# Kernel tuning notes

Hardware: AMD Instinct MI355X
Metric: run time of the kernel (lower is better)

The kernel has to match this reference:

```python
import jax, jax.numpy as jnp
import numpy as np

NUM_NODES = 50000
EMB_DIM = 128
PROJ_DIM = 768
HIDDEN = 256
NUM_REL = 16
NUM_BASES = 2
NUM_LAYERS = 3
NUM_EDGES = 400000
BN_EPS = 1e-5


def setup_inputs() -> dict:
    key = jax.random.key(0)
    ks = jax.random.split(key, 32)
    inp = {}
    inp["edge_index"] = jax.random.randint(ks[0], (2, NUM_EDGES), 0, NUM_NODES)
    inp["edge_type"] = jax.random.randint(ks[1], (NUM_EDGES,), 0, NUM_REL)
    inp["emb"] = jax.random.normal(ks[2], (NUM_NODES, EMB_DIM), jnp.float32)
    inp["proj_w"] = jax.random.normal(ks[3], (EMB_DIM, PROJ_DIM), jnp.float32) * 0.02
    inp["proj_b"] = jnp.zeros((PROJ_DIM,), jnp.float32)
    dims_in = [PROJ_DIM, HIDDEN, HIDDEN]
    for l in range(NUM_LAYERS):
        d_in = dims_in[l]
        k0, k1, k2 = jax.random.split(ks[4 + l], 3)
        inp[f"comp{l}"] = jax.random.normal(k0, (NUM_REL, NUM_BASES), jnp.float32)
        inp[f"bases{l}"] = jax.random.normal(k1, (NUM_BASES, d_in, HIDDEN), jnp.float32) * (1.0 / np.sqrt(d_in))
        inp[f"root{l}"] = jax.random.normal(k2, (d_in, HIDDEN), jnp.float32) * (1.0 / np.sqrt(d_in))
        inp[f"bias{l}"] = jnp.zeros((HIDDEN,), jnp.float32)
        inp[f"gamma{l}"] = jnp.ones((HIDDEN,), jnp.float32)
        inp[f"beta{l}"] = jnp.zeros((HIDDEN,), jnp.float32)
    return inp


def _rgcn_conv(x, src, dst, edge_type, comp, bases, root, bias):
    # Basis decomposition: W_r = sum_b comp[r,b] * bases[b]
    # Transform nodes per basis once: [B, N, out]
    h = jnp.einsum('nd,bdo->bno', x, bases)
    c = comp[edge_type]                         # [E, B]
    msg = jnp.einsum('beo,eb->eo', h[:, src, :], c)  # [E, out]
    # PyG RGCNConv uses mean aggregation per relation
    seg = dst * NUM_REL + edge_type             # combined (node, relation) id
    cnt = jax.ops.segment_sum(jnp.ones((msg.shape[0],), x.dtype), seg,
                              num_segments=NUM_NODES * NUM_REL)
    denom = jnp.maximum(cnt[seg], 1.0)
    agg = jax.ops.segment_sum(msg / denom[:, None], dst, num_segments=NUM_NODES)
    return agg + x @ root + bias


def _batchnorm(x, gamma, beta):
    mu = jnp.mean(x, axis=0)
    var = jnp.mean(jnp.square(x - mu), axis=0)  # biased, as in torch BN training
    return (x - mu) * jax.lax.rsqrt(var + BN_EPS) * gamma + beta


def reference(edge_index, edge_type, emb, proj_w, proj_b,
              comp0, bases0, root0, bias0, gamma0, beta0,
              comp1, bases1, root1, bias1, gamma1, beta1,
              comp2, bases2, root2, bias2, gamma2, beta2):
    src, dst = edge_index[0], edge_index[1]
    x = emb / jnp.maximum(jnp.linalg.norm(emb, axis=-1, keepdims=True), 1e-12)
    x = x @ proj_w + proj_b
    layers = [(comp0, bases0, root0, bias0, gamma0, beta0),
              (comp1, bases1, root1, bias1, gamma1, beta1),
              (comp2, bases2, root2, bias2, gamma2, beta2)]
    for (comp, bases, root, bias, gamma, beta) in layers:
        x = _rgcn_conv(x, src, dst, edge_type, comp, bases, root, bias)
        x = _batchnorm(x, gamma, beta)
        x = jax.nn.relu(x)
        # dropout: identity (eval mode / deterministic reference)
    return x
```

## Files before the change

kernel.cpp:

```cpp
#include <hip/hip_runtime.h>
#include <hip/hip_bf16.h>

#define NNODES 50000
#define NREL   16
#define NEDGE  400000
#define BN_EPS 1e-5f
#define M_REAL NNODES
#define MT256  196
#define SCAN_B 512
#define SCAN_NB ((NNODES + SCAN_B - 1) / SCAN_B)

typedef __attribute__((ext_vector_type(8))) short short8;
typedef __attribute__((ext_vector_type(4))) float f4;

__device__ __forceinline__ float bf2f(unsigned short u) {
    union { unsigned int i; float f; } x; x.i = ((unsigned int)u) << 16; return x.f;
}
__device__ __forceinline__ unsigned short f2bf(float f) {
    __hip_bfloat16 h = __float2bfloat16(f);
    union { __hip_bfloat16 h; unsigned short u; } x; x.h = h; return x.u;
}

__device__ __forceinline__ void g2l16(const unsigned short* g, unsigned short* l) {
    __builtin_amdgcn_global_load_lds(
        (const __attribute__((address_space(1))) unsigned int*)g,
        (__attribute__((address_space(3))) unsigned int*)l,
        16, 0, 0);
}

template<int K>
__global__ __launch_bounds__(512) void gemm3_k(
    const unsigned short* __restrict__ A,
    const unsigned short* __restrict__ WT,
    const float* __restrict__ bias,
    unsigned short* __restrict__ y,
    float* __restrict__ bns)
{
    const int tile_m = blockIdx.x * 256;

    __shared__ unsigned short As[2][256 * 64];
    __shared__ unsigned short Bs[2][256 * 64];

    const int w = threadIdx.x >> 6;
    const int l = threadIdx.x & 63;
    const int lm = l & 15;
    const int kq = l >> 4;
    const int wm = (w & 1) << 7;
    const int wn = (w >> 1) << 6;

    const int lrow = l >> 3;
    const int chunk = ((l & 7) + 8 - lrow) & 7;
    const unsigned short* srcA[4];
    const unsigned short* srcB[4];
    int dstoff[4];
#pragma unroll
    for (int it = 0; it < 4; ++it) {
        int rt = it * 64 + w * 8 + lrow;
        int rg = tile_m + rt; if (rg >= M_REAL) rg = M_REAL - 1;
        srcA[it] = A  + (size_t)rg * K + chunk * 8;
        srcB[it] = WT + (size_t)rt * K + chunk * 8;
        dstoff[it] = (it * 64 + w * 8) * 64;
    }

    unsigned aoff[8], boff[4];
#pragma unroll
    for (int mi = 0; mi < 8; ++mi)
        aoff[mi] = (unsigned)((wm + mi * 16 + lm) * 128 + (((kq + lm) & 7) << 4));
#pragma unroll
    for (int ni = 0; ni < 4; ++ni)
        boff[ni] = (unsigned)((wn + ni * 16 + lm) * 128 + (((kq + lm) & 7) << 4));

    f4 acc[8][4];
#pragma unroll
    for (int mi = 0; mi < 8; ++mi)
#pragma unroll
        for (int ni = 0; ni < 4; ++ni) acc[mi][ni] = (f4){0.f, 0.f, 0.f, 0.f};

#pragma unroll
    for (int it = 0; it < 4; ++it) {
        g2l16(srcA[it], As[0] + dstoff[it]);
        g2l16(srcB[it], Bs[0] + dstoff[it]);
    }
    __syncthreads();

    int cur = 0;
    for (int kc = 0; kc < K; kc += 64) {
        if (kc + 64 < K) {
#pragma unroll
            for (int it = 0; it < 4; ++it) {
                g2l16(srcA[it] + kc + 64, As[cur ^ 1] + dstoff[it]);
                g2l16(srcB[it] + kc + 64, Bs[cur ^ 1] + dstoff[it]);
            }
        }
#pragma unroll
        for (int kh = 0; kh < 2; ++kh) {
            const unsigned x = kh << 6;
            short8 af[8], bfr[4];
#pragma unroll
            for (int mi = 0; mi < 8; ++mi)
                af[mi] = *(const short8*)((const char*)As[cur] + (aoff[mi] ^ x));
#pragma unroll
            for (int ni = 0; ni < 4; ++ni)
                bfr[ni] = *(const short8*)((const char*)Bs[cur] + (boff[ni] ^ x));
#pragma unroll
            for (int mi = 0; mi < 8; ++mi)
#pragma unroll
                for (int ni = 0; ni < 4; ++ni)
                    acc[mi][ni] = __builtin_amdgcn_mfma_f32_16x16x32_bf16(
                        af[mi], bfr[ni], acc[mi][ni], 0, 0, 0);
        }
        __syncthreads();
        cur ^= 1;
    }

    int cols[4]; float bv[4];
#pragma unroll
    for (int ni = 0; ni < 4; ++ni) {
        cols[ni] = wn + ni * 16 + lm;
        bv[ni] = bias[cols[ni]];
    }
    float s1[4] = {0.f, 0.f, 0.f, 0.f}, s2[4] = {0.f, 0.f, 0.f, 0.f};
#pragma unroll
    for (int mi = 0; mi < 8; ++mi) {
#pragma unroll
        for (int rg = 0; rg < 4; ++rg) {
            int row = tile_m + wm + mi * 16 + kq * 4 + rg;
            if (row < M_REAL) {
                size_t base = (size_t)row * 256;
#pragma unroll
                for (int ni = 0; ni < 4; ++ni) {
                    float v = acc[mi][ni][rg] + bv[ni];
                    y[base + cols[ni]] = f2bf(v);
                    s1[ni] += v; s2[ni] += v * v;
                }
            }
        }
    }
#pragma unroll
    for (int ni = 0; ni < 4; ++ni) {
        float a = s1[ni], b = s2[ni];
        a += __shfl_xor(a, 16); a += __shfl_xor(a, 32);
        b += __shfl_xor(b, 16); b += __shfl_xor(b, 32);
        if (l < 16) {
            atomicAdd(&bns[cols[ni]], a);
            atomicAdd(&bns[256 + cols[ni]], b);
        }
    }
}

template<int D, bool HAST>
__global__ __launch_bounds__(256) void gatheru_k(
    unsigned short* buf, const float* __restrict__ comp,
    const unsigned int* __restrict__ rowptr, const float2* __restrict__ erec)
{
    constexpr int E = D / 64;
    constexpr int S = 3 * D + (HAST ? 64 : 0);
    __shared__ float scomp[32];
    if (threadIdx.x < 32) scomp[threadIdx.x] = comp[threadIdx.x];
    __syncthreads();
    int node = blockIdx.x * 4 + (threadIdx.x >> 6);
    int lane = threadIdx.x & 63;
    unsigned int p0 = rowptr[node], p1 = rowptr[node + 1];
    const unsigned short* xbase = buf + 2 * D + lane * E;

    float a0[E], a1[E], b0[E], b1[E];
#pragma unroll
    for (int e = 0; e < E; ++e) { a0[e] = a1[e] = b0[e] = b1[e] = 0.f; }
    float t0 = 0.f, t1 = 0.f;

    unsigned int p = p0;
    for (; p + 4 <= p1; p += 4) {
        float2 r[4];
        unsigned short v[4][E];
#pragma unroll
        for (int j = 0; j < 4; ++j) r[j] = erec[p + j];
#pragma unroll
        for (int j = 0; j < 4; ++j) {
            unsigned q = __float_as_uint(r[j].x);
            const unsigned short* s = xbase + (size_t)(q >> 4) * S;
            if (E == 2) { ushort2 t = *(const ushort2*)s; v[j][0] = t.x; v[j][1] = t.y; }
            else        { ushort4 t = *(const ushort4*)s; v[j][0] = t.x; v[j][1] = t.y;
                          v[j][2] = t.z; v[j][3] = t.w; }
        }
#pragma unroll
        for (int j = 0; j < 4; ++j) {
            unsigned q = __float_as_uint(r[j].x);
            float w0 = scomp[(q & 15) * 2] * r[j].y;
            float w1 = scomp[(q & 15) * 2 + 1] * r[j].y;
            if (HAST) { t0 += w0; t1 += w1; }
            float* d0 = (j & 1) ? b0 : a0;
            float* d1 = (j & 1) ? b1 : a1;
#pragma unroll
            for (int e = 0; e < E; ++e) {
                float xv = bf2f(v[j][e]);
                d0[e] += w0 * xv;
                d1[e] += w1 * xv;
            }
        }
    }
    for (; p < p1; ++p) {
        float2 r = erec[p];
        unsigned q = __float_as_uint(r.x);
        const unsigned short* s = xbase + (size_t)(q >> 4) * S;
        unsigned short v[E];
        if (E == 2) { ushort2 t = *(const ushort2*)s; v[0] = t.x; v[1] = t.y; }
        else        { ushort4 t = *(const ushort4*)s; v[0] = t.x; v[1] = t.y;
                      v[2] = t.z; v[3] = t.w; }
        float w0 = scomp[(q & 15) * 2] * r.y;
        float w1 = scomp[(q & 15) * 2 + 1] * r.y;
        if (HAST) { t0 += w0; t1 += w1; }
#pragma unroll
        for (int e = 0; e < E; ++e) {
            float xv = bf2f(v[e]);
            a0[e] += w0 * xv;
            a1[e] += w1 * xv;
        }
    }

    unsigned short* orow = buf + (size_t)node * S;
    if (E == 2) {
        ushort2 o0, o1;
        o0.x = f2bf(a0[0] + b0[0]); o0.y = f2bf(a0[1] + b0[1]);
        o1.x = f2bf(a1[0] + b1[0]); o1.y = f2bf(a1[1] + b1[1]);
        *(ushort2*)(orow + lane * 2) = o0;
        *(ushort2*)(orow + D + lane * 2) = o1;
    } else {
        ushort4 o0, o1;
        o0.x = f2bf(a0[0] + b0[0]); o0.y = f2bf(a0[1] + b0[1]);
        o0.z = f2bf(a0[2] + b0[2]); o0.w = f2bf(a0[3] + b0[3]);
        o1.x = f2bf(a1[0] + b1[0]); o1.y = f2bf(a1[1] + b1[1]);
        o1.z = f2bf(a1[2] + b1[2]); o1.w = f2bf(a1[3] + b1[3]);
        *(ushort4*)(orow + lane * 4) = o0;
        *(ushort4*)(orow + D + lane * 4) = o1;
    }
    if (HAST) {
        unsigned short tv = (lane == 0) ? f2bf(t0) : (lane == 1) ? f2bf(t1) : (unsigned short)0;
        orow[3 * D + lane] = tv;
    }
}

__global__ __launch_bounds__(256) void norm_k(const float* __restrict__ emb,
                                              unsigned short* __restrict__ buf)
{
    int node = blockIdx.x * 4 + (threadIdx.x >> 6);
    int lane = threadIdx.x & 63;
    const float2* p = (const float2*)(emb + (size_t)node * 128);
    float2 v = p[lane];
    float ss = v.x * v.x + v.y * v.y;
#pragma unroll
    for (int o = 32; o > 0; o >>= 1) ss += __shfl_xor(ss, o);
    float inv = 1.f / fmaxf(sqrtf(ss), 1e-12f);
    unsigned short* row = buf + (size_t)node * 448 + 256;
    unsigned int pack = (unsigned int)f2bf(v.x * inv) | ((unsigned int)f2bf(v.y * inv) << 16);
    ((unsigned int*)row)[lane] = pack;
}

__global__ void zero_k(unsigned int* __restrict__ cnt, unsigned int* __restrict__ cntd,
                       unsigned int* __restrict__ cursor, float* __restrict__ bns)
{
    int i = blockIdx.x * 256 + threadIdx.x;
    if (i < 800000) cnt[i] = 0u;
    if (i < 50000) { cntd[i] = 0u; cursor[i] = 0u; }
    if (i < 1536) bns[i] = 0.f;
}

__global__ void cnt_k(const int* __restrict__ ei, const int* __restrict__ et,
                      unsigned int* __restrict__ cnt, unsigned int* __restrict__ cntd)
{
    int e = blockIdx.x * 256 + threadIdx.x;
    if (e >= NEDGE) return;
    int dst = ei[NEDGE + e];
    atomicAdd(&cnt[(size_t)dst * NREL + et[e]], 1u);
    atomicAdd(&cntd[dst], 1u);
}

__global__ __launch_bounds__(SCAN_B) void scan1_k(const unsigned int* __restrict__ cntd,
                                                  unsigned int* __restrict__ partial,
                                                  unsigned int* __restrict__ bsum)
{
    __shared__ unsigned int s[SCAN_B];
    int i = blockIdx.x * SCAN_B + threadIdx.x;
    unsigned int v = (i < NNODES) ? cntd[i] : 0u;
    s[threadIdx.x] = v;
    __syncthreads();
    for (int off = 1; off < SCAN_B; off <<= 1) {
        unsigned int t = (threadIdx.x >= off) ? s[threadIdx.x - off] : 0u;
        __syncthreads();
        s[threadIdx.x] += t;
        __syncthreads();
    }
    if (i < NNODES) partial[i] = s[threadIdx.x];
    if (threadIdx.x == SCAN_B - 1) bsum[blockIdx.x] = s[SCAN_B - 1];
}

__global__ __launch_bounds__(128) void scan2_k(unsigned int* __restrict__ bsum)
{
    __shared__ unsigned int s[128];
    unsigned int v = (threadIdx.x < SCAN_NB) ? bsum[threadIdx.x] : 0u;
    s[threadIdx.x] = v;
    __syncthreads();
    for (int off = 1; off < 128; off <<= 1) {
        unsigned int t = (threadIdx.x >= off) ? s[threadIdx.x - off] : 0u;
        __syncthreads();
        s[threadIdx.x] += t;
        __syncthreads();
    }
    if (threadIdx.x < SCAN_NB) bsum[threadIdx.x] = s[threadIdx.x];
}

__global__ __launch_bounds__(SCAN_B) void scan3_k(const unsigned int* __restrict__ partial,
                                                  const unsigned int* __restrict__ bsum,
                                                  unsigned int* __restrict__ rowptr)
{
    int i = blockIdx.x * SCAN_B + threadIdx.x;
    if (i >= NNODES) return;
    unsigned int off = (blockIdx.x > 0) ? bsum[blockIdx.x - 1] : 0u;
    rowptr[i + 1] = partial[i] + off;
    if (i == 0) rowptr[0] = 0u;
}

__global__ void fill_k(const int* __restrict__ ei, const int* __restrict__ et,
                       const unsigned int* __restrict__ cnt,
                       const unsigned int* __restrict__ rowptr,
                       unsigned int* __restrict__ cursor,
                       float2* __restrict__ erec)
{
    int e = blockIdx.x * 256 + threadIdx.x;
    if (e >= NEDGE) return;
    int dst = ei[NEDGE + e];
    int t = et[e];
    unsigned int c = cnt[(size_t)dst * NREL + t];
    unsigned int pos = rowptr[dst] + atomicAdd(&cursor[dst], 1u);
    float2 r;
    r.x = __uint_as_float(((unsigned)ei[e] << 4) | (unsigned)t);
    r.y = 1.f / (float)(c ? c : 1u);
    erec[pos] = r;
}

__global__ __launch_bounds__(128) void pt_k(const float* __restrict__ proj_w,
                                            float* __restrict__ PT)
{
    int j = blockIdx.x, d = threadIdx.x;
    PT[(size_t)j * 128 + d] = proj_w[(size_t)d * 768 + j];
}

__global__ __launch_bounds__(128) void pm_k(
    const float* __restrict__ PT, const float* __restrict__ pb,
    const float* __restrict__ b0, const float* __restrict__ r0,
    const float* __restrict__ bias0,
    unsigned short* __restrict__ wTm0, float* __restrict__ biasM0)
{
    __shared__ float sw[128];
    __shared__ float spb[128];
    __shared__ float red[2];
    int seg = blockIdx.x >> 8;
    int n = blockIdx.x & 255;
    int d = threadIdx.x;
    float acc = 0.f, accb = 0.f;
    for (int ch = 0; ch < 6; ++ch) {
        int j0 = ch * 128;
        __syncthreads();
        int j = j0 + d;
        float wv;
        if (seg == 0)      wv = b0[(size_t)j * 256 + n];
        else if (seg == 1) wv = b0[768 * 256 + (size_t)j * 256 + n];
        else               wv = r0[(size_t)j * 256 + n];
        sw[d] = wv;
        spb[d] = pb[j];
        __syncthreads();
#pragma unroll 8
        for (int jj = 0; jj < 128; ++jj)
            acc += PT[(size_t)(j0 + jj) * 128 + d] * sw[jj];
        accb += spb[d] * sw[d];
    }
    for (int o = 32; o > 0; o >>= 1) accb += __shfl_xor(accb, o);
    if ((d & 63) == 0) red[d >> 6] = accb;
    __syncthreads();
    float tb = red[0] + red[1];
    wTm0[(size_t)n * 448 + seg * 128 + d] = f2bf(acc);
    if (seg == 0) { if (d == 0) wTm0[(size_t)n * 448 + 384] = f2bf(tb); }
    else if (seg == 1) { if (d == 0) wTm0[(size_t)n * 448 + 385] = f2bf(tb); }
    else {
        if (d == 0) biasM0[n] = tb + bias0[n];
        if (d >= 2 && d < 64) wTm0[(size_t)n * 448 + 384 + d] = 0;
    }
}

__global__ __launch_bounds__(256) void prep_k(
    const float* __restrict__ b1, const float* __restrict__ r1, const float* __restrict__ bias1,
    const float* __restrict__ b2, const float* __restrict__ r2, const float* __restrict__ bias2,
    unsigned short* __restrict__ wTm1, unsigned short* __restrict__ wTm2,
    float* __restrict__ biasM1, float* __restrict__ biasM2)
{
    int b = blockIdx.x;
    int n = threadIdx.x;
    if (b < 1536) {
        int layer = b / 768;
        int rem = b % 768;
        int seg = rem / 256;
        int k = rem % 256;
        const float* bb = layer ? b2 : b1;
        const float* rr = layer ? r2 : r1;
        const float* in = (seg < 2) ? (bb + (size_t)seg * 256 * 256) : rr;
        unsigned short* out = layer ? wTm2 : wTm1;
        out[(size_t)n * 768 + seg * 256 + k] = f2bf(in[(size_t)k * 256 + n]);
    } else {
        int layer = b - 1536;
        float* bm = layer ? biasM2 : biasM1;
        const float* bs = layer ? bias2 : bias1;
        bm[n] = bs[n];
    }
}

template<bool LAST>
__global__ __launch_bounds__(256) void apply_k(const unsigned short* __restrict__ y,
                                               const float* __restrict__ bns,
                                               const float* __restrict__ gamma,
                                               const float* __restrict__ beta,
                                               unsigned short* __restrict__ xn,
                                               float* __restrict__ outp)
{
    __shared__ float scsh[512];
    {
        const float inv_m = 1.f / (float)M_REAL;
        int c = threadIdx.x;
        float m1 = bns[c] * inv_m;
        float var = fmaxf(bns[256 + c] * inv_m - m1 * m1, 0.f);
        float inv = rsqrtf(var + BN_EPS);
        float sc = gamma[c] * inv;
        scsh[c] = sc;
        scsh[256 + c] = beta[c] - m1 * sc;
    }
    __syncthreads();

    int i = blockIdx.x * 256 + threadIdx.x;
    int row = i >> 5;
    int c8 = (i & 31) * 8;
    short8 v = *(const short8*)(y + (size_t)row * 256 + c8);
    f4 sca = *(const f4*)&scsh[c8];
    f4 scb = *(const f4*)&scsh[c8 + 4];
    f4 sha = *(const f4*)&scsh[256 + c8];
    f4 shb = *(const f4*)&scsh[256 + c8 + 4];
    float o0 = fmaxf(bf2f((unsigned short)v[0]) * sca.x + sha.x, 0.f);
    float o1 = fmaxf(bf2f((unsigned short)v[1]) * sca.y + sha.y, 0.f);
    float o2 = fmaxf(bf2f((unsigned short)v[2]) * sca.z + sha.z, 0.f);
    float o3 = fmaxf(bf2f((unsigned short)v[3]) * sca.w + sha.w, 0.f);
    float o4 = fmaxf(bf2f((unsigned short)v[4]) * scb.x + shb.x, 0.f);
    float o5 = fmaxf(bf2f((unsigned short)v[5]) * scb.y + shb.y, 0.f);
    float o6 = fmaxf(bf2f((unsigned short)v[6]) * scb.z + shb.z, 0.f);
    float o7 = fmaxf(bf2f((unsigned short)v[7]) * scb.w + shb.w, 0.f);
    if (LAST) {
        f4 w0 = {o0, o1, o2, o3};
        f4 w1 = {o4, o5, o6, o7};
        float* dst = outp + (size_t)row * 256 + c8;
        *(f4*)dst = w0;
        *(f4*)(dst + 4) = w1;
    } else {
        short8 u;
        u[0] = (short)f2bf(o0); u[1] = (short)f2bf(o1);
        u[2] = (short)f2bf(o2); u[3] = (short)f2bf(o3);
        u[4] = (short)f2bf(o4); u[5] = (short)f2bf(o5);
        u[6] = (short)f2bf(o6); u[7] = (short)f2bf(o7);
        *(short8*)(xn + (size_t)row * 768 + 512 + c8) = u;
    }
}

extern "C" void kernel_launch(void* const* d_in, const int* in_sizes, int n_in,
                              void* d_out, int out_size, void* d_ws, size_t ws_size,
                              hipStream_t stream)
{
    const int*   edge_index = (const int*)d_in[0];
    const int*   edge_type  = (const int*)d_in[1];
    const float* emb    = (const float*)d_in[2];
    const float* proj_w = (const float*)d_in[3];
    const float* proj_b = (const float*)d_in[4];
    const float* comp[3]  = {(const float*)d_in[5],  (const float*)d_in[11], (const float*)d_in[17]};
    const float* bases[3] = {(const float*)d_in[6],  (const float*)d_in[12], (const float*)d_in[18]};
    const float* root[3]  = {(const float*)d_in[7],  (const float*)d_in[13], (const float*)d_in[19]};
    const float* biasp[3] = {(const float*)d_in[8],  (const float*)d_in[14], (const float*)d_in[20]};
    const float* gamma[3] = {(const float*)d_in[9],  (const float*)d_in[15], (const float*)d_in[21]};
    const float* beta[3]  = {(const float*)d_in[10], (const float*)d_in[16], (const float*)d_in[22]};

    char* ws = (char*)d_ws;
    size_t off = 0;
    auto alloc = [&](size_t bytes) -> char* {
        char* p = ws + off;
        off = (off + bytes + 255) & ~(size_t)255;
        return p;
    };

    unsigned short* axl0 = (unsigned short*)alloc((size_t)NNODES * 448 * 2);
    unsigned short* axl1 = (unsigned short*)alloc((size_t)NNODES * 768 * 2);
    unsigned short* axl2 = (unsigned short*)alloc((size_t)NNODES * 768 * 2);
    unsigned short* y    = (unsigned short*)alloc((size_t)NNODES * 256 * 2);
    unsigned int*   cnt  = (unsigned int*)alloc((size_t)NNODES * NREL * 4);
    unsigned int*   cntd = (unsigned int*)alloc((size_t)NNODES * 4);
    unsigned int*   rowptr = (unsigned int*)alloc((size_t)(NNODES + 1) * 4);
    unsigned int*   cursor = (unsigned int*)alloc((size_t)NNODES * 4);
    unsigned int*   partial = (unsigned int*)alloc((size_t)NNODES * 4);
    unsigned int*   bsum = (unsigned int*)alloc(128 * 4);
    float2*         erec = (float2*)alloc((size_t)NEDGE * 8);
    float*          PT   = (float*)alloc((size_t)768 * 128 * 4);
    unsigned short* wTm0 = (unsigned short*)alloc((size_t)256 * 448 * 2);
    unsigned short* wTm1 = (unsigned short*)alloc((size_t)256 * 768 * 2);
    unsigned short* wTm2 = (unsigned short*)alloc((size_t)256 * 768 * 2);
    float* biasM = (float*)alloc(3 * 256 * 4);
    float* bns   = (float*)alloc(3 * 512 * 4);

    zero_k<<<3125, 256, 0, stream>>>(cnt, cntd, cursor, bns);
    norm_k<<<NNODES / 4, 256, 0, stream>>>(emb, axl0);
    cnt_k<<<(NEDGE + 255) / 256, 256, 0, stream>>>(edge_index, edge_type, cnt, cntd);
    scan1_k<<<SCAN_NB, SCAN_B, 0, stream>>>(cntd, partial, bsum);
    scan2_k<<<1, 128, 0, stream>>>(bsum);
    scan3_k<<<SCAN_NB, SCAN_B, 0, stream>>>(partial, bsum, rowptr);
    fill_k<<<(NEDGE + 255) / 256, 256, 0, stream>>>(edge_index, edge_type, cnt, rowptr,
                                                    cursor, erec);

    pt_k<<<768, 128, 0, stream>>>(proj_w, PT);
    pm_k<<<768, 128, 0, stream>>>(PT, proj_b, bases[0], root[0], biasp[0], wTm0, biasM);
    prep_k<<<1538, 256, 0, stream>>>(bases[1], root[1], biasp[1],
                                     bases[2], root[2], biasp[2],
                                     wTm1, wTm2, biasM + 256, biasM + 512);

    gatheru_k<128, true><<<NNODES / 4, 256, 0, stream>>>(axl0, comp[0], rowptr, erec);
    gemm3_k<448><<<MT256, 512, 0, stream>>>(axl0, wTm0, biasM, y, bns);
    apply_k<false><<<(NNODES * 32) / 256, 256, 0, stream>>>(y, bns, gamma[0], beta[0],
                                                            axl1, nullptr);

    gatheru_k<256, false><<<NNODES / 4, 256, 0, stream>>>(axl1, comp[1], rowptr, erec);
    gemm3_k<768><<<MT256, 512, 0, stream>>>(axl1, wTm1, biasM + 256, y, bns + 512);
    apply_k<false><<<(NNODES * 32) / 256, 256, 0, stream>>>(y, bns + 512, gamma[1], beta[1],
                                                            axl2, nullptr);

    gatheru_k<256, false><<<NNODES / 4, 256, 0, stream>>>(axl2, comp[2], rowptr, erec);
    gemm3_k<768><<<MT256, 512, 0, stream>>>(axl2, wTm2, biasM + 512, y, bns + 1024);
    apply_k<true><<<(NNODES * 32) / 256, 256, 0, stream>>>(y, bns + 1024, gamma[2], beta[2],
                                                           nullptr, (float*)d_out);
}
```

Baseline: 483.5 us.

## Merge setup kernels into fewer launches and unroll gather loop by eight

Several small setup kernels (zeroing, embedding normalisation, weight transpose, layer-1/2 weight prep) are fused into one multi-role init kernel, and edge counting is fused with the layer-0 projection-weight fold. The per-node degree array and its atomics are dropped; degrees are instead recomputed in the scan by summing the 16 per-relation counts. The gather loop also gains an 8-wide unrolled stage to keep more loads in flight. The aim is to cut launch count and atomics, at the cost of higher register pressure in the gather and blocks whose roles differ within the fused kernels.

```diff
diff --git a/kernel.cpp b/kernel.cpp
--- a/kernel.cpp
+++ b/kernel.cpp
@@ -169,6 +169,35 @@
     float t0 = 0.f, t1 = 0.f;
 
     unsigned int p = p0;
+    for (; p + 8 <= p1; p += 8) {
+        float2 r[8];
+        unsigned short v[8][E];
+#pragma unroll
+        for (int j = 0; j < 8; ++j) r[j] = erec[p + j];
+#pragma unroll
+        for (int j = 0; j < 8; ++j) {
+            unsigned q = __float_as_uint(r[j].x);
+            const unsigned short* s = xbase + (size_t)(q >> 4) * S;
+            if (E == 2) { ushort2 t = *(const ushort2*)s; v[j][0] = t.x; v[j][1] = t.y; }
+            else        { ushort4 t = *(const ushort4*)s; v[j][0] = t.x; v[j][1] = t.y;
+                          v[j][2] = t.z; v[j][3] = t.w; }
+        }
+#pragma unroll
+        for (int j = 0; j < 8; ++j) {
+            unsigned q = __float_as_uint(r[j].x);
+            float w0 = scomp[(q & 15) * 2] * r[j].y;
+            float w1 = scomp[(q & 15) * 2 + 1] * r[j].y;
+            if (HAST) { t0 += w0; t1 += w1; }
+            float* d0 = (j & 1) ? b0 : a0;
+            float* d1 = (j & 1) ? b1 : a1;
+#pragma unroll
+            for (int e = 0; e < E; ++e) {
+                float xv = bf2f(v[j][e]);
+                d0[e] += w0 * xv;
+                d1[e] += w1 * xv;
+            }
+        }
+    }
     for (; p + 4 <= p1; p += 4) {
         float2 r[4];
         unsigned short v[4][E];
@@ -239,160 +268,46 @@
     }
 }
 
-__global__ __launch_bounds__(256) void norm_k(const float* __restrict__ emb,
-                                              unsigned short* __restrict__ buf)
-{
-    int node = blockIdx.x * 4 + (threadIdx.x >> 6);
-    int lane = threadIdx.x & 63;
-    const float2* p = (const float2*)(emb + (size_t)node * 128);
-    float2 v = p[lane];
-    float ss = v.x * v.x + v.y * v.y;
-#pragma unroll
-    for (int o = 32; o > 0; o >>= 1) ss += __shfl_xor(ss, o);
-    float inv = 1.f / fmaxf(sqrtf(ss), 1e-12f);
-    unsigned short* row = buf + (size_t)node * 448 + 256;
-    unsigned int pack = (unsigned int)f2bf(v.x * inv) | ((unsigned int)f2bf(v.y * inv) << 16);
-    ((unsigned int*)row)[lane] = pack;
-}
-
-__global__ void zero_k(unsigned int* __restrict__ cnt, unsigned int* __restrict__ cntd,
-                       unsigned int* __restrict__ cursor, float* __restrict__ bns)
-{
-    int i = blockIdx.x * 256 + threadIdx.x;
-    if (i < 800000) cnt[i] = 0u;
-    if (i < 50000) { cntd[i] = 0u; cursor[i] = 0u; }
-    if (i < 1536) bns[i] = 0.f;
-}
-
-__global__ void cnt_k(const int* __restrict__ ei, const int* __restrict__ et,
-                      unsigned int* __restrict__ cnt, unsigned int* __restrict__ cntd)
-{
-    int e = blockIdx.x * 256 + threadIdx.x;
-    if (e >= NEDGE) return;
-    int dst = ei[NEDGE + e];
-    atomicAdd(&cnt[(size_t)dst * NREL + et[e]], 1u);
-    atomicAdd(&cntd[dst], 1u);
-}
-
-__global__ __launch_bounds__(SCAN_B) void scan1_k(const unsigned int* __restrict__ cntd,
-                                                  unsigned int* __restrict__ partial,
-                                                  unsigned int* __restrict__ bsum)
-{
-    __shared__ unsigned int s[SCAN_B];
-    int i = blockIdx.x * SCAN_B + threadIdx.x;
-    unsigned int v = (i < NNODES) ? cntd[i] : 0u;
-    s[threadIdx.x] = v;
-    __syncthreads();
-    for (int off = 1; off < SCAN_B; off <<= 1) {
-        unsigned int t = (threadIdx.x >= off) ? s[threadIdx.x - off] : 0u;
-        __syncthreads();
-        s[threadIdx.x] += t;
-        __syncthreads();
-    }
-    if (i < NNODES) partial[i] = s[threadIdx.x];
-    if (threadIdx.x == SCAN_B - 1) bsum[blockIdx.x] = s[SCAN_B - 1];
-}
-
-__global__ __launch_bounds__(128) void scan2_k(unsigned int* __restrict__ bsum)
-{
-    __shared__ unsigned int s[128];
-    unsigned int v = (threadIdx.x < SCAN_NB) ? bsum[threadIdx.x] : 0u;
-    s[threadIdx.x] = v;
-    __syncthreads();
-    for (int off = 1; off < 128; off <<= 1) {
-        unsigned int t = (threadIdx.x >= off) ? s[threadIdx.x - off] : 0u;
-        __syncthreads();
-        s[threadIdx.x] += t;
-        __syncthreads();
-    }
-    if (threadIdx.x < SCAN_NB) bsum[threadIdx.x] = s[threadIdx.x];
-}
-
-__global__ __launch_bounds__(SCAN_B) void scan3_k(const unsigned int* __restrict__ partial,
-                                                  const unsigned int* __restrict__ bsum,
-                                                  unsigned int* __restrict__ rowptr)
-{
-    int i = blockIdx.x * SCAN_B + threadIdx.x;
-    if (i >= NNODES) return;
-    unsigned int off = (blockIdx.x > 0) ? bsum[blockIdx.x - 1] : 0u;
-    rowptr[i + 1] = partial[i] + off;
-    if (i == 0) rowptr[0] = 0u;
-}
-
-__global__ void fill_k(const int* __restrict__ ei, const int* __restrict__ et,
-                       const unsigned int* __restrict__ cnt,
-                       const unsigned int* __restrict__ rowptr,
-                       unsigned int* __restrict__ cursor,
-                       float2* __restrict__ erec)
-{
-    int e = blockIdx.x * 256 + threadIdx.x;
-    if (e >= NEDGE) return;
-    int dst = ei[NEDGE + e];
-    int t = et[e];
-    unsigned int c = cnt[(size_t)dst * NREL + t];
-    unsigned int pos = rowptr[dst] + atomicAdd(&cursor[dst], 1u);
-    float2 r;
-    r.x = __uint_as_float(((unsigned)ei[e] << 4) | (unsigned)t);
-    r.y = 1.f / (float)(c ? c : 1u);
-    erec[pos] = r;
-}
-
-__global__ __launch_bounds__(128) void pt_k(const float* __restrict__ proj_w,
-                                            float* __restrict__ PT)
-{
-    int j = blockIdx.x, d = threadIdx.x;
-    PT[(size_t)j * 128 + d] = proj_w[(size_t)d * 768 + j];
-}
-
-__global__ __launch_bounds__(128) void pm_k(
-    const float* __restrict__ PT, const float* __restrict__ pb,
-    const float* __restrict__ b0, const float* __restrict__ r0,
-    const float* __restrict__ bias0,
-    unsigned short* __restrict__ wTm0, float* __restrict__ biasM0)
-{
-    __shared__ float sw[128];
-    __shared__ float spb[128];
-    __shared__ float red[2];
-    int seg = blockIdx.x >> 8;
-    int n = blockIdx.x & 255;
-    int d = threadIdx.x;
-    float acc = 0.f, accb = 0.f;
-    for (int ch = 0; ch < 6; ++ch) {
-        int j0 = ch * 128;
-        __syncthreads();
-        int j = j0 + d;
-        float wv;
-        if (seg == 0)      wv = b0[(size_t)j * 256 + n];
-        else if (seg == 1) wv = b0[768 * 256 + (size_t)j * 256 + n];
-        else               wv = r0[(size_t)j * 256 + n];
-        sw[d] = wv;
-        spb[d] = pb[j];
-        __syncthreads();
-#pragma unroll 8
-        for (int jj = 0; jj < 128; ++jj)
-            acc += PT[(size_t)(j0 + jj) * 128 + d] * sw[jj];
-        accb += spb[d] * sw[d];
-    }
-    for (int o = 32; o > 0; o >>= 1) accb += __shfl_xor(accb, o);
-    if ((d & 63) == 0) red[d >> 6] = accb;
-    __syncthreads();
-    float tb = red[0] + red[1];
-    wTm0[(size_t)n * 448 + seg * 128 + d] = f2bf(acc);
-    if (seg == 0) { if (d == 0) wTm0[(size_t)n * 448 + 384] = f2bf(tb); }
-    else if (seg == 1) { if (d == 0) wTm0[(size_t)n * 448 + 385] = f2bf(tb); }
-    else {
-        if (d == 0) biasM0[n] = tb + bias0[n];
-        if (d >= 2 && d < 64) wTm0[(size_t)n * 448 + 384 + d] = 0;
-    }
-}
-
-__global__ __launch_bounds__(256) void prep_k(
-    const float* __restrict__ b1, const float* __restrict__ r1, const float* __restrict__ bias1,
-    const float* __restrict__ b2, const float* __restrict__ r2, const float* __restrict__ bias2,
+__global__ __launch_bounds__(256) void init_k(
+    unsigned int* __restrict__ cnt, unsigned int* __restrict__ cursor,
+    float* __restrict__ bns,
+    const float* __restrict__ emb, unsigned short* __restrict__ buf,
+    const float* __restrict__ proj_w, float* __restrict__ PT,
+    const float* __restrict__ b1, const float* __restrict__ r1,
+    const float* __restrict__ b2, const float* __restrict__ r2,
+    const float* __restrict__ bias1, const float* __restrict__ bias2,
     unsigned short* __restrict__ wTm1, unsigned short* __restrict__ wTm2,
     float* __restrict__ biasM1, float* __restrict__ biasM2)
 {
-    int b = blockIdx.x;
+    if (blockIdx.x < 3125) {
+        int i = blockIdx.x * 256 + threadIdx.x;
+        if (i < 800000) cnt[i] = 0u;
+        if (i < 50000) cursor[i] = 0u;
+        if (i < 1536) bns[i] = 0.f;
+        return;
+    }
+    if (blockIdx.x < 15625) {
+        int node = (blockIdx.x - 3125) * 4 + (threadIdx.x >> 6);
+        int lane = threadIdx.x & 63;
+        const float2* p = (const float2*)(emb + (size_t)node * 128);
+        float2 v = p[lane];
+        float ss = v.x * v.x + v.y * v.y;
+#pragma unroll
+        for (int o = 32; o > 0; o >>= 1) ss += __shfl_xor(ss, o);
+        float inv = 1.f / fmaxf(sqrtf(ss), 1e-12f);
+        unsigned short* row = buf + (size_t)node * 448 + 256;
+        unsigned int pack = (unsigned int)f2bf(v.x * inv) | ((unsigned int)f2bf(v.y * inv) << 16);
+        ((unsigned int*)row)[lane] = pack;
+        return;
+    }
+    int b = blockIdx.x - 15625;
+    if (b < 384) {
+        int j = b * 2 + (threadIdx.x >> 7);
+        int d = threadIdx.x & 127;
+        PT[(size_t)j * 128 + d] = proj_w[(size_t)d * 768 + j];
+        return;
+    }
+    b -= 384;
     int n = threadIdx.x;
     if (b < 1536) {
         int layer = b / 768;
@@ -410,6 +325,133 @@
         const float* bs = layer ? bias2 : bias1;
         bm[n] = bs[n];
     }
+}
+
+__global__ __launch_bounds__(256) void cntpm_k(
+    const int* __restrict__ ei, const int* __restrict__ et,
+    unsigned int* __restrict__ cnt,
+    const float* __restrict__ PT, const float* __restrict__ pb,
+    const float* __restrict__ b0, const float* __restrict__ r0,
+    const float* __restrict__ bias0,
+    unsigned short* __restrict__ wTm0, float* __restrict__ biasM0)
+{
+    if (blockIdx.x < 1563) {
+        int e = blockIdx.x * 256 + threadIdx.x;
+        if (e >= NEDGE) return;
+        int dst = ei[NEDGE + e];
+        atomicAdd(&cnt[(size_t)dst * NREL + et[e]], 1u);
+        return;
+    }
+    __shared__ float sw[128];
+    __shared__ float spb[128];
+    __shared__ float red[4];
+    int pmb = blockIdx.x - 1563;
+    int seg = pmb >> 8;
+    int n = pmb & 255;
+    int d = threadIdx.x;
+    float acc = 0.f, accb = 0.f;
+    for (int ch = 0; ch < 6; ++ch) {
+        int j0 = ch * 128;
+        __syncthreads();
+        if (d < 128) {
+            int j = j0 + d;
+            float wv;
+            if (seg == 0)      wv = b0[(size_t)j * 256 + n];
+            else if (seg == 1) wv = b0[768 * 256 + (size_t)j * 256 + n];
+            else               wv = r0[(size_t)j * 256 + n];
+            sw[d] = wv;
+            spb[d] = pb[j];
+        }
+        __syncthreads();
+        if (d < 128) {
+#pragma unroll 8
+            for (int jj = 0; jj < 128; ++jj)
+                acc += PT[(size_t)(j0 + jj) * 128 + d] * sw[jj];
+            accb += spb[d] * sw[d];
+        }
+    }
+    for (int o = 32; o > 0; o >>= 1) accb += __shfl_xor(accb, o);
+    if ((d & 63) == 0) red[d >> 6] = accb;
+    __syncthreads();
+    float tb = red[0] + red[1];
+    if (d < 128) {
+        wTm0[(size_t)n * 448 + seg * 128 + d] = f2bf(acc);
+        if (seg == 0) { if (d == 0) wTm0[(size_t)n * 448 + 384] = f2bf(tb); }
+        else if (seg == 1) { if (d == 0) wTm0[(size_t)n * 448 + 385] = f2bf(tb); }
+        else {
+            if (d == 0) biasM0[n] = tb + bias0[n];
+            if (d >= 2 && d < 64) wTm0[(size_t)n * 448 + 384 + d] = 0;
+        }
+    }
+}
+
+__global__ __launch_bounds__(SCAN_B) void scan1_k(const unsigned int* __restrict__ cnt,
+                                                  unsigned int* __restrict__ partial,
+                                                  unsigned int* __restrict__ bsum)
+{
+    __shared__ unsigned int s[SCAN_B];
+    int i = blockIdx.x * SCAN_B + threadIdx.x;
+    unsigned int v = 0u;
+    if (i < NNODES) {
+        const uint4* cp = (const uint4*)(cnt + (size_t)i * 16);
+        uint4 c0 = cp[0], c1 = cp[1], c2 = cp[2], c3 = cp[3];
+        v = c0.x + c0.y + c0.z + c0.w + c1.x + c1.y + c1.z + c1.w
+          + c2.x + c2.y + c2.z + c2.w + c3.x + c3.y + c3.z + c3.w;
+    }
+    s[threadIdx.x] = v;
+    __syncthreads();
+    for (int off = 1; off < SCAN_B; off <<= 1) {
+        unsigned int t = (threadIdx.x >= off) ? s[threadIdx.x - off] : 0u;
+        __syncthreads();
+        s[threadIdx.x] += t;
+        __syncthreads();
+    }
+    if (i < NNODES) partial[i] = s[threadIdx.x];
+    if (threadIdx.x == SCAN_B - 1) bsum[blockIdx.x] = s[SCAN_B - 1];
+}
+
+__global__ __launch_bounds__(128) void scan2_k(unsigned int* __restrict__ bsum)
+{
+    __shared__ unsigned int s[128];
+    unsigned int v = (threadIdx.x < SCAN_NB) ? bsum[threadIdx.x] : 0u;
+    s[threadIdx.x] = v;
+    __syncthreads();
+    for (int off = 1; off < 128; off <<= 1) {
+        unsigned int t = (threadIdx.x >= off) ? s[threadIdx.x - off] : 0u;
+        __syncthreads();
+        s[threadIdx.x] += t;
+        __syncthreads();
+    }
+    if (threadIdx.x < SCAN_NB) bsum[threadIdx.x] = s[threadIdx.x];
+}
+
+__global__ __launch_bounds__(SCAN_B) void scan3_k(const unsigned int* __restrict__ partial,
+                                                  const unsigned int* __restrict__ bsum,
+                                                  unsigned int* __restrict__ rowptr)
+{
+    int i = blockIdx.x * SCAN_B + threadIdx.x;
+    if (i >= NNODES) return;
+    unsigned int off = (blockIdx.x > 0) ? bsum[blockIdx.x - 1] : 0u;
+    rowptr[i + 1] = partial[i] + off;
+    if (i == 0) rowptr[0] = 0u;
+}
+
+__global__ void fill_k(const int* __restrict__ ei, const int* __restrict__ et,
+                       const unsigned int* __restrict__ cnt,
+                       const unsigned int* __restrict__ rowptr,
+                       unsigned int* __restrict__ cursor,
+                       float2* __restrict__ erec)
+{
+    int e = blockIdx.x * 256 + threadIdx.x;
+    if (e >= NEDGE) return;
+    int dst = ei[NEDGE + e];
+    int t = et[e];
+    unsigned int c = cnt[(size_t)dst * NREL + t];
+    unsigned int pos = rowptr[dst] + atomicAdd(&cursor[dst], 1u);
+    float2 r;
+    r.x = __uint_as_float(((unsigned)ei[e] << 4) | (unsigned)t);
+    r.y = 1.f / (float)(c ? c : 1u);
+    erec[pos] = r;
 }
 
 template<bool LAST>
@@ -494,7 +536,6 @@
     unsigned short* axl2 = (unsigned short*)alloc((size_t)NNODES * 768 * 2);
     unsigned short* y    = (unsigned short*)alloc((size_t)NNODES * 256 * 2);
     unsigned int*   cnt  = (unsigned int*)alloc((size_t)NNODES * NREL * 4);
-    unsigned int*   cntd = (unsigned int*)alloc((size_t)NNODES * 4);
     unsigned int*   rowptr = (unsigned int*)alloc((size_t)(NNODES + 1) * 4);
     unsigned int*   cursor = (unsigned int*)alloc((size_t)NNODES * 4);
     unsigned int*   partial = (unsigned int*)alloc((size_t)NNODES * 4);
@@ -507,21 +548,20 @@
     float* biasM = (float*)alloc(3 * 256 * 4);
     float* bns   = (float*)alloc(3 * 512 * 4);
 
-    zero_k<<<3125, 256, 0, stream>>>(cnt, cntd, cursor, bns);
-    norm_k<<<NNODES / 4, 256, 0, stream>>>(emb, axl0);
-    cnt_k<<<(NEDGE + 255) / 256, 256, 0, stream>>>(edge_index, edge_type, cnt, cntd);
-    scan1_k<<<SCAN_NB, SCAN_B, 0, stream>>>(cntd, partial, bsum);
+    init_k<<<17547, 256, 0, stream>>>(cnt, cursor, bns, emb, axl0,
+                                      proj_w, PT,
+                                      bases[1], root[1], bases[2], root[2],
+                                      biasp[1], biasp[2],
+                                      wTm1, wTm2, biasM + 256, biasM + 512);
+    cntpm_k<<<2331, 256, 0, stream>>>(edge_index, edge_type, cnt,
+                                      PT, proj_b, bases[0], root[0], biasp[0],
+                                      wTm0, biasM);
+    scan1_k<<<SCAN_NB, SCAN_B, 0, stream>>>(cnt, partial, bsum);
     scan2_k<<<1, 128, 0, stream>>>(bsum);
     scan3_k<<<SCAN_NB, SCAN_B, 0, stream>>>(partial, bsum, rowptr);
     fill_k<<<(NEDGE + 255) / 256, 256, 0, stream>>>(edge_index, edge_type, cnt, rowptr,
                                                     cursor, erec);
 
-    pt_k<<<768, 128, 0, stream>>>(proj_w, PT);
-    pm_k<<<768, 128, 0, stream>>>(PT, proj_b, bases[0], root[0], biasp[0], wTm0, biasM);
-    prep_k<<<1538, 256, 0, stream>>>(bases[1], root[1], biasp[1],
-                                     bases[2], root[2], biasp[2],
-                                     wTm1, wTm2, biasM + 256, biasM + 512);
-
     gatheru_k<128, true><<<NNODES / 4, 256, 0, stream>>>(axl0, comp[0], rowptr, erec);
     gemm3_k<448><<<MT256, 512, 0, stream>>>(axl0, wTm0, biasM, y, bns);
     apply_k<false><<<(NNODES * 32) / 256, 256, 0, stream>>>(y, bns, gamma[0], beta[0],
```

Result: faster. 461.7 us (-4.5%).
